# Optimization experiments

Hardware: AMD Instinct MI355X
Metric: run time of the kernel (lower is better)

Reference implementation:

```python
import jax, jax.numpy as jnp
import numpy as np

N = 30000          # nodes
E = 480000         # directed edges (avg degree 16)
F_IN = 376         # num_features (hard-coded in module)
HID = 512          # nhid (hard-coded)
NEG_SLOPE = 0.2    # PyG GATConv default negative_slope


def _lin(k, fi, fo):
    return (jax.random.normal(k, (fi, fo), jnp.float32) / np.sqrt(fi)).astype(jnp.float32)


def setup_inputs() -> dict:
    key = jax.random.key(0)
    ks = jax.random.split(key, 16)
    d = {}
    d["x"] = jax.random.normal(ks[0], (N, F_IN), jnp.float32)
    d["edge_index"] = jax.random.randint(ks[1], (2, E), 0, N)
    d["edge_weight"] = jax.random.uniform(ks[2], (E,), jnp.float32)
    # GCNConv(376,512) and GCNConv(512,512)
    d["W1"] = _lin(ks[3], F_IN, HID); d["b1"] = jnp.zeros((HID,), jnp.float32)
    d["W2"] = _lin(ks[4], HID, HID);  d["b2"] = jnp.zeros((HID,), jnp.float32)
    # SAGEConv(512,512): lin_l on aggregated neighbors, lin_r on root
    d["sage_Wl"] = _lin(ks[5], HID, HID)
    d["sage_Wr"] = _lin(ks[6], HID, HID)
    d["sage_b"] = jnp.zeros((HID,), jnp.float32)
    # GATConv(1536, 1, heads=4, concat=False)
    d["gat1_W"] = _lin(ks[7], 3 * HID, 4)
    d["gat1_a_src"] = jax.random.normal(ks[8], (4,), jnp.float32) * 0.1
    d["gat1_a_dst"] = jax.random.normal(ks[9], (4,), jnp.float32) * 0.1
    d["gat1_b"] = jnp.zeros((1,), jnp.float32)
    # GATConv(1536, 1, heads=16, concat=False)
    d["gat2_W"] = _lin(ks[10], 3 * HID, 16)
    d["gat2_a_src"] = jax.random.normal(ks[11], (16,), jnp.float32) * 0.1
    d["gat2_a_dst"] = jax.random.normal(ks[12], (16,), jnp.float32) * 0.1
    d["gat2_b"] = jnp.zeros((1,), jnp.float32)
    return d


def gcn_conv(x, src, dst, ew, W, b, n):
    # PyG GCNConv: add self-loops (weight 1), symmetric normalization
    loop = jnp.arange(n)
    s = jnp.concatenate([src, loop])
    t = jnp.concatenate([dst, loop])
    w = jnp.concatenate([ew, jnp.ones((n,), ew.dtype)])
    deg = jax.ops.segment_sum(w, t, num_segments=n)
    dinv = jnp.where(deg > 0, jax.lax.rsqrt(deg), 0.0)
    norm = dinv[s] * w * dinv[t]                       # [E+N]
    h = x @ W                                           # [N, out]
    out = jax.ops.segment_sum(norm[:, None] * h[s], t, num_segments=n)
    return out + b


def sage_conv(x, src, dst, Wl, Wr, b, n):
    # PyG SAGEConv: mean neighbor aggregation + root transform
    sums = jax.ops.segment_sum(x[src], dst, num_segments=n)
    cnt = jax.ops.segment_sum(jnp.ones((src.shape[0],), x.dtype), dst, num_segments=n)
    mean = sums / jnp.maximum(cnt, 1.0)[:, None]
    return mean @ Wl + x @ Wr + b


def gat_conv(x, src, dst, W, a_src, a_dst, b, n):
    # PyG GATConv (out_channels=1, concat=False -> mean over heads), self-loops added
    loop = jnp.arange(n)
    s = jnp.concatenate([src, loop])
    t = jnp.concatenate([dst, loop])
    h = x @ W                                           # [N, heads] (C=1)
    e = jax.nn.leaky_relu(h[s] * a_src + h[t] * a_dst, NEG_SLOPE)  # [E+N, heads]
    m = jax.ops.segment_max(e, t, num_segments=n)       # stable segment softmax
    ex = jnp.exp(e - m[t])
    den = jax.ops.segment_sum(ex, t, num_segments=n)
    alpha = ex / den[t]
    out = jax.ops.segment_sum(alpha * h[s], t, num_segments=n)     # [N, heads]
    return out.mean(axis=1, keepdims=True) + b          # [N, 1]


def reference(x, edge_index, edge_weight, W1, b1, W2, b2,
              sage_Wl, sage_Wr, sage_b,
              gat1_W, gat1_a_src, gat1_a_dst, gat1_b,
              gat2_W, gat2_a_src, gat2_a_dst, gat2_b):
    n = x.shape[0]
    src, dst = edge_index[0], edge_index[1]
    x1 = jax.nn.relu(gcn_conv(x, src, dst, edge_weight, W1, b1, n))
    x2 = jax.nn.relu(gcn_conv(x1, src, dst, edge_weight, W2, b2, n))
    x3 = jax.nn.relu(sage_conv(x1, src, dst, sage_Wl, sage_Wr, sage_b, n))
    dense_features = jnp.concatenate([x1, x2, x3], axis=1)  # [N, 1536]
    a1 = gat_conv(dense_features, src, dst, gat1_W, gat1_a_src, gat1_a_dst, gat1_b, n)
    a2 = gat_conv(dense_features, src, dst, gat2_W, gat2_a_src, gat2_a_dst, gat2_b, n)
    x_out = jnp.ravel((a1 + a2) * 0.5)                  # [N]
    return x_out, dense_features
```

## Files before the change

kernel.cpp:

```cpp
#include <hip/hip_runtime.h>
#include <hip/hip_bf16.h>
#include <stdint.h>

#define N_NODES 30000
#define M_PAD   30080
#define N_EDGES 480000
#define F_IN 376
#define K1   384
#define HID 512
#define DENSE_F 1536
#define NHEADS 20
#define HG_LD 32

typedef __bf16 bf16_t;
typedef bf16_t bf16x8 __attribute__((ext_vector_type(8)));
typedef float  f32x4  __attribute__((ext_vector_type(4)));

#define S1 (512 * K1)
#define S2 (512 * 512)
#define S3 (512 * 1024)
#define S4 (128 * DENSE_F)
#define PW_ELEMS (S1 + S2 + S3 + S4 + NHEADS)

#define EB_BLOCKS ((N_EDGES + 255) / 256)
#define CX_BLOCKS ((M_PAD * K1) / 256)
#define PW_BLOCKS ((PW_ELEMS + 255) / 256)
#define PRO_BLOCKS (EB_BLOCKS + CX_BLOCKS + PW_BLOCKS)

__global__ __launch_bounds__(256) void prologue(
    const int* __restrict__ dst, const float* __restrict__ ew,
    float* __restrict__ deg, int* __restrict__ cnt,
    const float* __restrict__ x, bf16_t* __restrict__ xb,
    const float* __restrict__ W1, const float* __restrict__ W2,
    const float* __restrict__ Wl, const float* __restrict__ Wr,
    const float* __restrict__ g1W, const float* __restrict__ g2W,
    const float* __restrict__ a1s, const float* __restrict__ a1d,
    const float* __restrict__ a2s, const float* __restrict__ a2d,
    bf16_t* __restrict__ W1t, bf16_t* __restrict__ W2t,
    bf16_t* __restrict__ Bst, bf16_t* __restrict__ Wgt,
    float* __restrict__ asrc, float* __restrict__ adst)
{
    int b = blockIdx.x;
    if (b < EB_BLOCKS) {
        int e = b * 256 + threadIdx.x;
        if (e >= N_EDGES) return;
        int t = dst[e];
        atomicAdd(&deg[t], ew[e]);
        atomicAdd(&cnt[t], 1);
    } else if (b < EB_BLOCKS + CX_BLOCKS) {
        int tid = (b - EB_BLOCKS) * 256 + threadIdx.x;
        int r = tid / K1, c = tid - r * K1;
        float v = (r < N_NODES && c < F_IN) ? x[r * F_IN + c] : 0.f;
        xb[tid] = (bf16_t)v;
    } else {
        int tid = (b - EB_BLOCKS - CX_BLOCKS) * 256 + threadIdx.x;
        if (tid < S1) {
            int n = tid / K1, k = tid - n * K1;
            W1t[tid] = (bf16_t)((k < F_IN) ? W1[k * HID + n] : 0.f);
        } else if (tid < S1 + S2) {
            int t = tid - S1;
            int n = t >> 9, k = t & 511;
            W2t[t] = (bf16_t)W2[k * HID + n];
        } else if (tid < S1 + S2 + S3) {
            int t = tid - S1 - S2;
            int n = t >> 10, k = t & 1023;
            Bst[t] = (bf16_t)((k < HID) ? Wl[k * HID + n] : Wr[(k - HID) * HID + n]);
        } else if (tid < S1 + S2 + S3 + S4) {
            int t = tid - S1 - S2 - S3;
            int n = t / DENSE_F, k = t - n * DENSE_F;
            float v = (n < 4) ? g1W[k * 4 + n] : (n < NHEADS) ? g2W[k * 16 + (n - 4)] : 0.f;
            Wgt[t] = (bf16_t)v;
        } else if (tid < S1 + S2 + S3 + S4 + NHEADS) {
            int hh = tid - S1 - S2 - S3 - S4;
            asrc[hh] = (hh < 4) ? a1s[hh] : a2s[hh - 4];
            adst[hh] = (hh < 4) ? a1d[hh] : a2d[hh - 4];
        }
    }
}

#define SEG 30
__global__ __launch_bounds__(1024) void scan_rowptr_fast(
    const int* __restrict__ cnt, int* __restrict__ rowptr, int* __restrict__ woff,
    float* __restrict__ deg, float* __restrict__ dinv)
{
    int t = threadIdx.x;
    int base = t * SEG;
    int v[SEG];
    int sum = 0;
#pragma unroll
    for (int j = 0; j < SEG; ++j) {
        int i = base + j;
        int c = (i < N_NODES) ? cnt[i] : 0;
        v[j] = c;
        sum += c;
        if (i < N_NODES) {
            float d = deg[i] + 1.0f;
            deg[i] = d;
            dinv[i] = rsqrtf(d);
        }
    }
    int lane = t & 63;
    int wid = t >> 6;
    int s = sum;
#pragma unroll
    for (int off = 1; off < 64; off <<= 1) {
        int u = __shfl_up(s, off);
        if (lane >= off) s += u;
    }
    __shared__ int wsum[16];
    if (lane == 63) wsum[wid] = s;
    __syncthreads();
    if (t < 16) {
        int ws = wsum[t];
#pragma unroll
        for (int off = 1; off < 16; off <<= 1) {
            int u = __shfl_up(ws, off);
            if (t >= off) ws += u;
        }
        wsum[t] = ws;
    }
    __syncthreads();
    int carry = (wid > 0) ? wsum[wid - 1] : 0;
    int excl = carry + s - sum;
#pragma unroll
    for (int j = 0; j < SEG; ++j) {
        int i = base + j;
        if (i < N_NODES) { rowptr[i] = excl; woff[i] = excl; }
        excl += v[j];
    }
    if (t == 1023) rowptr[N_NODES] = excl;
}

__global__ __launch_bounds__(256) void scatter_csr(
    const int* __restrict__ src, const int* __restrict__ dst,
    const float* __restrict__ ew, int* __restrict__ woff,
    int* __restrict__ col, float* __restrict__ wcsr)
{
    int e = blockIdx.x * 256 + threadIdx.x;
    if (e >= N_EDGES) return;
    int t = dst[e];
    int p = atomicAdd(&woff[t], 1);
    col[p] = src[e];
    wcsr[p] = ew[e];
}

__global__ __launch_bounds__(256) void gemm_bf16(
    const bf16_t* __restrict__ A1, int lda1, int ksplit,
    const bf16_t* __restrict__ A2, int lda2,
    const bf16_t* __restrict__ Bt, int ldb,
    float* __restrict__ C, bf16_t* __restrict__ Cb, long ldc, int K,
    const float* __restrict__ bias, int ncols, int accum)
{
    __shared__ bf16_t As[128 * 32];
    __shared__ bf16_t Bs[128 * 32];
    const int tid = threadIdx.x;
    const int wid = tid >> 6, lane = tid & 63;
    const int li = lane & 15, kq = lane >> 4;
    const int wm = (wid >> 1) * 64, wn = (wid & 1) * 64;
    const long r0 = (long)blockIdx.y * 128;
    const int  n0 = blockIdx.x * 128;

    const int kb = K / (int)gridDim.z;
    const int k_lo = (int)blockIdx.z * kb;
    const int k_hi = k_lo + kb;

    f32x4 acc[4][4] = {};

    const int s0 = wid * 64 + lane;
    const int s1 = 256 + s0;
    const int am0 = s0 >> 2, ak0 = (s0 & 3) ^ ((am0 >> 1) & 3);
    const int am1 = s1 >> 2, ak1 = (s1 & 3) ^ ((am1 >> 1) & 3);
    const int swz = (li >> 1) & 3;

    for (int k0 = k_lo; k0 < k_hi; k0 += 32) {
        const bf16_t* Ab; int lda;
        if (k0 < ksplit) { Ab = A1 + k0;            lda = lda1; }
        else             { Ab = A2 + (k0 - ksplit); lda = lda2; }
        __builtin_amdgcn_global_load_lds(
            (const __attribute__((address_space(1))) void*)(Ab + (r0 + am0) * (long)lda + ak0 * 8),
            (__attribute__((address_space(3))) void*)(As + (wid * 64) * 8), 16, 0, 0);
        __builtin_amdgcn_global_load_lds(
            (const __attribute__((address_space(1))) void*)(Ab + (r0 + am1) * (long)lda + ak1 * 8),
            (__attribute__((address_space(3))) void*)(As + (256 + wid * 64) * 8), 16, 0, 0);
        __builtin_amdgcn_global_load_lds(
            (const __attribute__((address_space(1))) void*)(Bt + (n0 + am0) * (long)ldb + k0 + ak0 * 8),
            (__attribute__((address_space(3))) void*)(Bs + (wid * 64) * 8), 16, 0, 0);
        __builtin_amdgcn_global_load_lds(
            (const __attribute__((address_space(1))) void*)(Bt + (n0 + am1) * (long)ldb + k0 + ak1 * 8),
            (__attribute__((address_space(3))) void*)(Bs + (256 + wid * 64) * 8), 16, 0, 0);
        __syncthreads();

        bf16x8 a[4], b[4];
#pragma unroll
        for (int f = 0; f < 4; ++f) {
            int m = wm + f * 16 + li;
            a[f] = *(const bf16x8*)(As + m * 32 + ((kq ^ swz) * 8));
            int n = wn + f * 16 + li;
            b[f] = *(const bf16x8*)(Bs + n * 32 + ((kq ^ swz) * 8));
        }
#pragma unroll
        for (int fm = 0; fm < 4; ++fm)
#pragma unroll
            for (int fn = 0; fn < 4; ++fn)
                acc[fm][fn] = __builtin_amdgcn_mfma_f32_16x16x32_bf16(
                    a[fm], b[fn], acc[fm][fn], 0, 0, 0);
        __syncthreads();
    }

#pragma unroll
    for (int fm = 0; fm < 4; ++fm) {
#pragma unroll
        for (int r = 0; r < 4; ++r) {
            long row = r0 + wm + fm * 16 + kq * 4 + r;
            if (row >= N_NODES) continue;
#pragma unroll
            for (int fn = 0; fn < 4; ++fn) {
                int colg = n0 + wn + fn * 16 + li;
                if (colg >= ncols) continue;
                float v = acc[fm][fn][r];
                if (bias) v = fmaxf(v + bias[colg], 0.f);
                if (C) {
                    if (accum) atomicAdd(&C[row * ldc + colg], v);
                    else       C[row * ldc + colg] = v;
                }
                if (Cb) Cb[row * ldc + colg] = (bf16_t)v;
            }
        }
    }
}

__global__ __launch_bounds__(256) void agg_x(
    const bf16_t* __restrict__ xb, const int* __restrict__ rowptr,
    const int* __restrict__ col, const float* __restrict__ wcsr,
    const float* __restrict__ dinv, const float* __restrict__ deg,
    bf16_t* __restrict__ aggx)
{
    int i = blockIdx.x * 4 + (threadIdx.x >> 6);
    int lane = threadIdx.x & 63;
    int c = lane * 8;
    bool act = (c < K1);
    float di = dinv[i];
    float selfw = 1.0f / deg[i];
    float acc0[8] = {}, acc1[8] = {};
    if (act) {
        bf16x8 sv = *(const bf16x8*)(xb + (long)i * K1 + c);
#pragma unroll
        for (int j = 0; j < 8; ++j) acc0[j] = selfw * (float)sv[j];
    }
    int e = rowptr[i], e1 = rowptr[i + 1];
    for (; e + 1 < e1; e += 2) {
        int sA = col[e], sB = col[e + 1];
        float wA = dinv[sA] * wcsr[e] * di;
        float wB = dinv[sB] * wcsr[e + 1] * di;
        if (act) {
            bf16x8 vA = *(const bf16x8*)(xb + (long)sA * K1 + c);
            bf16x8 vB = *(const bf16x8*)(xb + (long)sB * K1 + c);
#pragma unroll
            for (int j = 0; j < 8; ++j) {
                acc0[j] = fmaf(wA, (float)vA[j], acc0[j]);
                acc1[j] = fmaf(wB, (float)vB[j], acc1[j]);
            }
        }
    }
    if (e < e1) {
        int sA = col[e];
        float wA = dinv[sA] * wcsr[e] * di;
        if (act) {
            bf16x8 vA = *(const bf16x8*)(xb + (long)sA * K1 + c);
#pragma unroll
            for (int j = 0; j < 8; ++j) acc0[j] = fmaf(wA, (float)vA[j], acc0[j]);
        }
    }
    if (act) {
        bf16x8 ob;
#pragma unroll
        for (int j = 0; j < 8; ++j) ob[j] = (bf16_t)(acc0[j] + acc1[j]);
        *reinterpret_cast<bf16x8*>(aggx + (long)i * K1 + c) = ob;
    }
}

__global__ __launch_bounds__(256) void agg_x1(
    const bf16_t* __restrict__ x1b ,
    const int* __restrict__ rowptr, const int* __restrict__ col,
    const float* __restrict__ wcsr, const float* __restrict__ dinv,
    const float* __restrict__ deg, const int* __restrict__ cnt,
    bf16_t* __restrict__ gbf, bf16_t* __restrict__ meanb)
{
    int i = blockIdx.x * 4 + (threadIdx.x >> 6);
    int lane = threadIdx.x & 63;
    int c = lane * 8;
    float di = dinv[i];
    float selfw = 1.0f / deg[i];
    bf16x8 sv = *(const bf16x8*)(x1b + (long)i * DENSE_F + c);
    float g0[8], g1[8], m0[8], m1[8];
#pragma unroll
    for (int j = 0; j < 8; ++j) {
        g0[j] = selfw * (float)sv[j];
        g1[j] = 0.f; m0[j] = 0.f; m1[j] = 0.f;
    }
    int e = rowptr[i], e1 = rowptr[i + 1];
    for (; e + 1 < e1; e += 2) {
        int sA = col[e], sB = col[e + 1];
        float wA = dinv[sA] * wcsr[e] * di;
        float wB = dinv[sB] * wcsr[e + 1] * di;
        bf16x8 vA = *(const bf16x8*)(x1b + (long)sA * DENSE_F + c);
        bf16x8 vB = *(const bf16x8*)(x1b + (long)sB * DENSE_F + c);
#pragma unroll
        for (int j = 0; j < 8; ++j) {
            float fA = (float)vA[j], fB = (float)vB[j];
            g0[j] = fmaf(wA, fA, g0[j]);
            g1[j] = fmaf(wB, fB, g1[j]);
            m0[j] += fA;
            m1[j] += fB;
        }
    }
    if (e < e1) {
        int sA = col[e];
        float wA = dinv[sA] * wcsr[e] * di;
        bf16x8 vA = *(const bf16x8*)(x1b + (long)sA * DENSE_F + c);
#pragma unroll
        for (int j = 0; j < 8; ++j) {
            float fA = (float)vA[j];
            g0[j] = fmaf(wA, fA, g0[j]);
            m0[j] += fA;
        }
    }
    float inv = 1.0f / fmaxf((float)cnt[i], 1.0f);
    bf16x8 og, om;
#pragma unroll
    for (int j = 0; j < 8; ++j) {
        og[j] = (bf16_t)(g0[j] + g1[j]);
        om[j] = (bf16_t)((m0[j] + m1[j]) * inv);
    }
    *reinterpret_cast<bf16x8*>(gbf   + (long)i * HID + c) = og;
    *reinterpret_cast<bf16x8*>(meanb + (long)i * HID + c) = om;
}

__global__ __launch_bounds__(256) void gat_agg(
    const float* __restrict__ hgat, const int* __restrict__ rowptr,
    const int* __restrict__ col, const float* __restrict__ asrc,
    const float* __restrict__ adst, const float* __restrict__ b1p,
    const float* __restrict__ b2p, float* __restrict__ xout)
{
    int i = blockIdx.x * 4 + (threadIdx.x >> 6);
    int lane = threadIdx.x & 63;
    int h = (lane < NHEADS) ? lane : 0;
    float hg_i = hgat[(long)i * HG_LD + h];
    float as = asrc[h], ad = adst[h];
    float adhg = ad * hg_i;
    float ev = hg_i * as + adhg;
    ev = ev > 0.f ? ev : 0.2f * ev;
    float ex = __expf(ev);
    float den0 = ex, og0 = ex * hg_i, den1 = 0.f, og1 = 0.f;
    int e = rowptr[i], e1 = rowptr[i + 1];
    for (; e + 1 < e1; e += 2) {
        int sA = col[e], sB = col[e + 1];
        float hA = hgat[(long)sA * HG_LD + h];
        float hB = hgat[(long)sB * HG_LD + h];
        float tA = fmaf(hA, as, adhg); tA = tA > 0.f ? tA : 0.2f * tA;
        float tB = fmaf(hB, as, adhg); tB = tB > 0.f ? tB : 0.2f * tB;
        float xA = __expf(tA), xB = __expf(tB);
        den0 += xA; og0 = fmaf(xA, hA, og0);
        den1 += xB; og1 = fmaf(xB, hB, og1);
    }
    if (e < e1) {
        int sA = col[e];
        float hA = hgat[(long)sA * HG_LD + h];
        float tA = fmaf(hA, as, adhg); tA = tA > 0.f ? tA : 0.2f * tA;
        float xA = __expf(tA);
        den0 += xA; og0 = fmaf(xA, hA, og0);
    }
    float out = (lane < NHEADS) ? (og0 + og1) / (den0 + den1) : 0.f;
    float s4 = out + __shfl_xor(out, 1);
    s4 += __shfl_xor(s4, 2);
    float g0 = __shfl(s4, 0);
    float g1 = __shfl(s4, 4);
    float g2 = __shfl(s4, 8);
    float g3 = __shfl(s4, 12);
    float g4 = __shfl(s4, 16);
    if (lane == 0) {
        float a1 = g0 * 0.25f + b1p[0];
        float a2 = (g1 + g2 + g3 + g4) * 0.0625f + b2p[0];
        xout[i] = 0.5f * (a1 + a2);
    }
}

extern "C" void kernel_launch(void* const* d_in, const int* in_sizes, int n_in,
                              void* d_out, int out_size, void* d_ws, size_t ws_size,
                              hipStream_t stream) {
    (void)in_sizes; (void)n_in; (void)out_size; (void)ws_size;
    const float* x    = (const float*)d_in[0];
    const int*   ei   = (const int*)d_in[1];
    const float* ew   = (const float*)d_in[2];
    const float* W1   = (const float*)d_in[3];
    const float* b1   = (const float*)d_in[4];
    const float* W2   = (const float*)d_in[5];
    const float* b2   = (const float*)d_in[6];
    const float* sWl  = (const float*)d_in[7];
    const float* sWr  = (const float*)d_in[8];
    const float* sb   = (const float*)d_in[9];
    const float* g1W  = (const float*)d_in[10];
    const float* g1as = (const float*)d_in[11];
    const float* g1ad = (const float*)d_in[12];
    const float* g1b  = (const float*)d_in[13];
    const float* g2W  = (const float*)d_in[14];
    const float* g2as = (const float*)d_in[15];
    const float* g2ad = (const float*)d_in[16];
    const float* g2b  = (const float*)d_in[17];

    const int* src = ei;
    const int* dst = ei + N_EDGES;

    float* xout  = (float*)d_out;
    float* dense = xout + N_NODES;

    size_t off = 0;
    auto alloc = [&](size_t nbytes) -> void* {
        void* p = (char*)d_ws + off;
        off += (nbytes + 255) & ~(size_t)255;
        return p;
    };
    bf16_t* dense_bf = (bf16_t*)alloc((size_t)M_PAD * DENSE_F * 2);
    bf16_t* x_bf     = (bf16_t*)alloc((size_t)M_PAD * K1 * 2);
    bf16_t* aggx_bf  = (bf16_t*)alloc((size_t)M_PAD * K1 * 2);
    bf16_t* g_bf     = (bf16_t*)alloc((size_t)M_PAD * HID * 2);
    bf16_t* mean_bf  = (bf16_t*)alloc((size_t)M_PAD * HID * 2);
    float*  hgat     = (float*)alloc((size_t)M_PAD * HG_LD * 4);
    bf16_t* W1t      = (bf16_t*)alloc((size_t)512 * K1 * 2);
    bf16_t* W2t      = (bf16_t*)alloc((size_t)512 * 512 * 2);
    bf16_t* Bst      = (bf16_t*)alloc((size_t)512 * 1024 * 2);
    bf16_t* Wgt      = (bf16_t*)alloc((size_t)128 * DENSE_F * 2);
    float*  deg      = (float*)alloc((size_t)N_NODES * 4);
    float*  dinv     = (float*)alloc((size_t)N_NODES * 4);
    float*  asrc     = (float*)alloc(32 * 4);
    float*  adst     = (float*)alloc(32 * 4);
    int*    cnt      = (int*)alloc((size_t)N_NODES * 4);
    int*    rowp     = (int*)alloc((size_t)(N_NODES + 1) * 4);
    int*    woff     = (int*)alloc((size_t)N_NODES * 4);
    int*    colx     = (int*)alloc((size_t)N_EDGES * 4);
    float*  wcsr     = (float*)alloc((size_t)N_EDGES * 4);

    const int EB = EB_BLOCKS;

    hipMemsetAsync(deg, 0, (size_t)N_NODES * 4, stream);
    hipMemsetAsync(cnt, 0, (size_t)N_NODES * 4, stream);
    hipMemsetAsync(hgat, 0, (size_t)M_PAD * HG_LD * 4, stream);

    prologue<<<PRO_BLOCKS, 256, 0, stream>>>(
        dst, ew, deg, cnt, x, x_bf,
        W1, W2, sWl, sWr, g1W, g2W, g1as, g1ad, g2as, g2ad,
        W1t, W2t, Bst, Wgt, asrc, adst);
    scan_rowptr_fast<<<1, 1024, 0, stream>>>(cnt, rowp, woff, deg, dinv);
    scatter_csr<<<EB, 256, 0, stream>>>(src, dst, ew, woff, colx, wcsr);

    const dim3 gB(256);
    const dim3 g512(HID / 128, M_PAD / 128);
    const dim3 g128z(1, M_PAD / 128, 2);

    agg_x<<<N_NODES / 4, 256, 0, stream>>>(x_bf, rowp, colx, wcsr, dinv, deg, aggx_bf);
    gemm_bf16<<<g512, gB, 0, stream>>>(aggx_bf, K1, K1, aggx_bf, K1, W1t, K1,
                                       dense, dense_bf, DENSE_F, K1, b1, 512, 0);

    agg_x1<<<N_NODES / 4, 256, 0, stream>>>(dense_bf, rowp, colx, wcsr, dinv, deg, cnt,
                                            g_bf, mean_bf);
    gemm_bf16<<<g512, gB, 0, stream>>>(g_bf, HID, HID, g_bf, HID, W2t, HID,
                                       dense + HID, dense_bf + HID, DENSE_F,
                                       HID, b2, 512, 0);
    gemm_bf16<<<g512, gB, 0, stream>>>(mean_bf, HID, HID, dense_bf, DENSE_F,
                                       Bst, 1024, dense + 2 * HID,
                                       dense_bf + 2 * HID, DENSE_F, 1024, sb, 512, 0);

    gemm_bf16<<<g128z, gB, 0, stream>>>(dense_bf, DENSE_F, DENSE_F, dense_bf, DENSE_F,
                                        Wgt, DENSE_F, hgat, nullptr, HG_LD,
                                        DENSE_F, nullptr, HG_LD, 1);
    gat_agg<<<N_NODES / 4, 256, 0, stream>>>(hgat, rowp, colx, asrc, adst, g1b, g2b, xout);
}
```

Baseline: 837.7 us.

## Merge two independent GEMMs into one launch, unroll edge loops, drop split-K atomics

The GCN-layer-2 GEMM and the SAGE GEMM run as one dual-dispatch kernel, with block x selecting which problem to compute. This removes a launch and lets the two fill the GPU together. The GAT projection GEMM no longer uses split-K with atomicAdd, which also removes the hgat memset, at the cost of fewer blocks (235) for that GEMM. The three edge-aggregation kernels unroll their neighbor loops from 2 to 4 to put more gathers in flight.

```diff
diff --git a/kernel.cpp b/kernel.cpp
--- a/kernel.cpp
+++ b/kernel.cpp
@@ -144,25 +144,18 @@
     wcsr[p] = ew[e];
 }
 
-__global__ __launch_bounds__(256) void gemm_bf16(
+__device__ __forceinline__ void gemm_body(
     const bf16_t* __restrict__ A1, int lda1, int ksplit,
     const bf16_t* __restrict__ A2, int lda2,
     const bf16_t* __restrict__ Bt, int ldb,
     float* __restrict__ C, bf16_t* __restrict__ Cb, long ldc, int K,
-    const float* __restrict__ bias, int ncols, int accum)
-{
-    __shared__ bf16_t As[128 * 32];
-    __shared__ bf16_t Bs[128 * 32];
+    const float* __restrict__ bias, int ncols,
+    int n0, long r0, bf16_t* As, bf16_t* Bs)
+{
     const int tid = threadIdx.x;
     const int wid = tid >> 6, lane = tid & 63;
     const int li = lane & 15, kq = lane >> 4;
     const int wm = (wid >> 1) * 64, wn = (wid & 1) * 64;
-    const long r0 = (long)blockIdx.y * 128;
-    const int  n0 = blockIdx.x * 128;
-
-    const int kb = K / (int)gridDim.z;
-    const int k_lo = (int)blockIdx.z * kb;
-    const int k_hi = k_lo + kb;
 
     f32x4 acc[4][4] = {};
 
@@ -172,7 +165,7 @@
     const int am1 = s1 >> 2, ak1 = (s1 & 3) ^ ((am1 >> 1) & 3);
     const int swz = (li >> 1) & 3;
 
-    for (int k0 = k_lo; k0 < k_hi; k0 += 32) {
+    for (int k0 = 0; k0 < K; k0 += 32) {
         const bf16_t* Ab; int lda;
         if (k0 < ksplit) { Ab = A1 + k0;            lda = lda1; }
         else             { Ab = A2 + (k0 - ksplit); lda = lda2; }
@@ -219,13 +212,47 @@
                 if (colg >= ncols) continue;
                 float v = acc[fm][fn][r];
                 if (bias) v = fmaxf(v + bias[colg], 0.f);
-                if (C) {
-                    if (accum) atomicAdd(&C[row * ldc + colg], v);
-                    else       C[row * ldc + colg] = v;
-                }
+                if (C)  C[row * ldc + colg]  = v;
                 if (Cb) Cb[row * ldc + colg] = (bf16_t)v;
             }
         }
+    }
+}
+
+__global__ __launch_bounds__(256) void gemm_bf16(
+    const bf16_t* __restrict__ A1, int lda1, int ksplit,
+    const bf16_t* __restrict__ A2, int lda2,
+    const bf16_t* __restrict__ Bt, int ldb,
+    float* __restrict__ C, bf16_t* __restrict__ Cb, long ldc, int K,
+    const float* __restrict__ bias, int ncols)
+{
+    __shared__ bf16_t As[128 * 32];
+    __shared__ bf16_t Bs[128 * 32];
+    gemm_body(A1, lda1, ksplit, A2, lda2, Bt, ldb, C, Cb, ldc, K, bias, ncols,
+              blockIdx.x * 128, (long)blockIdx.y * 128, As, Bs);
+}
+
+__global__ __launch_bounds__(256) void gemm_bf16_dual(
+    const bf16_t* __restrict__ A1a, int lda1a, int ksplita,
+    const bf16_t* __restrict__ A2a, int lda2a,
+    const bf16_t* __restrict__ Bta, int ldba,
+    float* __restrict__ Ca, bf16_t* __restrict__ Cba, long ldca, int Ka,
+    const float* __restrict__ biasa, int ncolsa,
+    const bf16_t* __restrict__ A1b, int lda1b, int ksplitb,
+    const bf16_t* __restrict__ A2b, int lda2b,
+    const bf16_t* __restrict__ Btb, int ldbb,
+    float* __restrict__ Cb2, bf16_t* __restrict__ Cbb, long ldcb, int Kb,
+    const float* __restrict__ biasb, int ncolsb)
+{
+    __shared__ bf16_t As[128 * 32];
+    __shared__ bf16_t Bs[128 * 32];
+    long r0 = (long)blockIdx.y * 128;
+    if (blockIdx.x < 4) {
+        gemm_body(A1a, lda1a, ksplita, A2a, lda2a, Bta, ldba, Ca, Cba, ldca, Ka,
+                  biasa, ncolsa, blockIdx.x * 128, r0, As, Bs);
+    } else {
+        gemm_body(A1b, lda1b, ksplitb, A2b, lda2b, Btb, ldbb, Cb2, Cbb, ldcb, Kb,
+                  biasb, ncolsb, (blockIdx.x - 4) * 128, r0, As, Bs);
     }
 }
 
@@ -248,21 +275,27 @@
         for (int j = 0; j < 8; ++j) acc0[j] = selfw * (float)sv[j];
     }
     int e = rowptr[i], e1 = rowptr[i + 1];
-    for (; e + 1 < e1; e += 2) {
-        int sA = col[e], sB = col[e + 1];
-        float wA = dinv[sA] * wcsr[e] * di;
+    for (; e + 3 < e1; e += 4) {
+        int sA = col[e], sB = col[e + 1], sC = col[e + 2], sD = col[e + 3];
+        float wA = dinv[sA] * wcsr[e]     * di;
         float wB = dinv[sB] * wcsr[e + 1] * di;
+        float wC = dinv[sC] * wcsr[e + 2] * di;
+        float wD = dinv[sD] * wcsr[e + 3] * di;
         if (act) {
             bf16x8 vA = *(const bf16x8*)(xb + (long)sA * K1 + c);
             bf16x8 vB = *(const bf16x8*)(xb + (long)sB * K1 + c);
+            bf16x8 vC = *(const bf16x8*)(xb + (long)sC * K1 + c);
+            bf16x8 vD = *(const bf16x8*)(xb + (long)sD * K1 + c);
 #pragma unroll
             for (int j = 0; j < 8; ++j) {
                 acc0[j] = fmaf(wA, (float)vA[j], acc0[j]);
                 acc1[j] = fmaf(wB, (float)vB[j], acc1[j]);
+                acc0[j] = fmaf(wC, (float)vC[j], acc0[j]);
+                acc1[j] = fmaf(wD, (float)vD[j], acc1[j]);
             }
         }
     }
-    if (e < e1) {
+    for (; e < e1; ++e) {
         int sA = col[e];
         float wA = dinv[sA] * wcsr[e] * di;
         if (act) {
@@ -299,22 +332,29 @@
         g1[j] = 0.f; m0[j] = 0.f; m1[j] = 0.f;
     }
     int e = rowptr[i], e1 = rowptr[i + 1];
-    for (; e + 1 < e1; e += 2) {
-        int sA = col[e], sB = col[e + 1];
-        float wA = dinv[sA] * wcsr[e] * di;
+    for (; e + 3 < e1; e += 4) {
+        int sA = col[e], sB = col[e + 1], sC = col[e + 2], sD = col[e + 3];
+        float wA = dinv[sA] * wcsr[e]     * di;
         float wB = dinv[sB] * wcsr[e + 1] * di;
+        float wC = dinv[sC] * wcsr[e + 2] * di;
+        float wD = dinv[sD] * wcsr[e + 3] * di;
         bf16x8 vA = *(const bf16x8*)(x1b + (long)sA * DENSE_F + c);
         bf16x8 vB = *(const bf16x8*)(x1b + (long)sB * DENSE_F + c);
+        bf16x8 vC = *(const bf16x8*)(x1b + (long)sC * DENSE_F + c);
+        bf16x8 vD = *(const bf16x8*)(x1b + (long)sD * DENSE_F + c);
 #pragma unroll
         for (int j = 0; j < 8; ++j) {
             float fA = (float)vA[j], fB = (float)vB[j];
+            float fC = (float)vC[j], fD = (float)vD[j];
             g0[j] = fmaf(wA, fA, g0[j]);
             g1[j] = fmaf(wB, fB, g1[j]);
-            m0[j] += fA;
-            m1[j] += fB;
-        }
-    }
-    if (e < e1) {
+            g0[j] = fmaf(wC, fC, g0[j]);
+            g1[j] = fmaf(wD, fD, g1[j]);
+            m0[j] += fA + fC;
+            m1[j] += fB + fD;
+        }
+    }
+    for (; e < e1; ++e) {
         int sA = col[e];
         float wA = dinv[sA] * wcsr[e] * di;
         bf16x8 vA = *(const bf16x8*)(x1b + (long)sA * DENSE_F + c);
@@ -353,17 +393,24 @@
     float ex = __expf(ev);
     float den0 = ex, og0 = ex * hg_i, den1 = 0.f, og1 = 0.f;
     int e = rowptr[i], e1 = rowptr[i + 1];
-    for (; e + 1 < e1; e += 2) {
-        int sA = col[e], sB = col[e + 1];
+    for (; e + 3 < e1; e += 4) {
+        int sA = col[e], sB = col[e + 1], sC = col[e + 2], sD = col[e + 3];
         float hA = hgat[(long)sA * HG_LD + h];
         float hB = hgat[(long)sB * HG_LD + h];
+        float hC = hgat[(long)sC * HG_LD + h];
+        float hD = hgat[(long)sD * HG_LD + h];
         float tA = fmaf(hA, as, adhg); tA = tA > 0.f ? tA : 0.2f * tA;
         float tB = fmaf(hB, as, adhg); tB = tB > 0.f ? tB : 0.2f * tB;
+        float tC = fmaf(hC, as, adhg); tC = tC > 0.f ? tC : 0.2f * tC;
+        float tD = fmaf(hD, as, adhg); tD = tD > 0.f ? tD : 0.2f * tD;
         float xA = __expf(tA), xB = __expf(tB);
+        float xC = __expf(tC), xD = __expf(tD);
         den0 += xA; og0 = fmaf(xA, hA, og0);
         den1 += xB; og1 = fmaf(xB, hB, og1);
-    }
-    if (e < e1) {
+        den0 += xC; og0 = fmaf(xC, hC, og0);
+        den1 += xD; og1 = fmaf(xD, hD, og1);
+    }
+    for (; e < e1; ++e) {
         int sA = col[e];
         float hA = hgat[(long)sA * HG_LD + h];
         float tA = fmaf(hA, as, adhg); tA = tA > 0.f ? tA : 0.2f * tA;
@@ -444,7 +491,6 @@
 
     hipMemsetAsync(deg, 0, (size_t)N_NODES * 4, stream);
     hipMemsetAsync(cnt, 0, (size_t)N_NODES * 4, stream);
-    hipMemsetAsync(hgat, 0, (size_t)M_PAD * HG_LD * 4, stream);
 
     prologue<<<PRO_BLOCKS, 256, 0, stream>>>(
         dst, ew, deg, cnt, x, x_bf,
@@ -455,23 +501,23 @@
 
     const dim3 gB(256);
     const dim3 g512(HID / 128, M_PAD / 128);
-    const dim3 g128z(1, M_PAD / 128, 2);
+    const dim3 gdual(8, M_PAD / 128);
+    const dim3 g128(1, M_PAD / 128);
 
     agg_x<<<N_NODES / 4, 256, 0, stream>>>(x_bf, rowp, colx, wcsr, dinv, deg, aggx_bf);
     gemm_bf16<<<g512, gB, 0, stream>>>(aggx_bf, K1, K1, aggx_bf, K1, W1t, K1,
-                                       dense, dense_bf, DENSE_F, K1, b1, 512, 0);
+                                       dense, dense_bf, DENSE_F, K1, b1, 512);
 
     agg_x1<<<N_NODES / 4, 256, 0, stream>>>(dense_bf, rowp, colx, wcsr, dinv, deg, cnt,
                                             g_bf, mean_bf);
-    gemm_bf16<<<g512, gB, 0, stream>>>(g_bf, HID, HID, g_bf, HID, W2t, HID,
-                                       dense + HID, dense_bf + HID, DENSE_F,
-                                       HID, b2, 512, 0);
-    gemm_bf16<<<g512, gB, 0, stream>>>(mean_bf, HID, HID, dense_bf, DENSE_F,
-                                       Bst, 1024, dense + 2 * HID,
-                                       dense_bf + 2 * HID, DENSE_F, 1024, sb, 512, 0);
-
-    gemm_bf16<<<g128z, gB, 0, stream>>>(dense_bf, DENSE_F, DENSE_F, dense_bf, DENSE_F,
-                                        Wgt, DENSE_F, hgat, nullptr, HG_LD,
-                                        DENSE_F, nullptr, HG_LD, 1);
+    gemm_bf16_dual<<<gdual, gB, 0, stream>>>(
+        g_bf, HID, HID, g_bf, HID, W2t, HID,
+        dense + HID, dense_bf + HID, DENSE_F, HID, b2, 512,
+        mean_bf, HID, HID, dense_bf, DENSE_F, Bst, 1024,
+        dense + 2 * HID, dense_bf + 2 * HID, DENSE_F, 1024, sb, 512);
+
+    gemm_bf16<<<g128, gB, 0, stream>>>(dense_bf, DENSE_F, DENSE_F, dense_bf, DENSE_F,
+                                       Wgt, DENSE_F, hgat, nullptr, HG_LD,
+                                       DENSE_F, nullptr, HG_LD);
     gat_agg<<<N_NODES / 4, 256, 0, stream>>>(hgat, rowp, colx, asrc, adst, g1b, g2b, xout);
 }
```

Result: no change. 828.3 us (-1.1%).
